# Performance work log

Measured on AMD Instinct MI355X. Metric: run time of the kernel, lower is better.

Reference implementation:

```python
import jax, jax.numpy as jnp
import numpy as np

NUM_QUBITS = 512
NUM_CORES = 16
CORE_SIZE = 64
HIDDEN = 128
BATCH = 2048


def setup_inputs() -> dict:
    key = jax.random.key(0)
    k1, k2, k3 = jax.random.split(key, 3)
    last_assignment = jax.random.randint(k1, (BATCH, NUM_QUBITS), 0, NUM_CORES, dtype=jnp.int32)
    adjacency = jnp.ones((NUM_CORES, NUM_CORES), dtype=jnp.float32)  # all-to-all core graph
    qubit_embedding = jax.random.normal(k2, (NUM_QUBITS + 1, HIDDEN), dtype=jnp.float32)
    gcn_weight = jax.random.normal(k3, (HIDDEN, HIDDEN), dtype=jnp.float32) * (1.0 / np.sqrt(HIDDEN))
    gcn_bias = jnp.zeros((HIDDEN,), dtype=jnp.float32)
    return {
        'last_assignment': last_assignment,
        'adjacency': adjacency,
        'qubit_embedding': qubit_embedding,
        'gcn_weight': gcn_weight,
        'gcn_bias': gcn_bias,
    }


def reference(last_assignment, adjacency, qubit_embedding, gcn_weight, gcn_bias):
    B, Q = last_assignment.shape
    C = adjacency.shape[0]
    # --- replace the sequential per-qubit scatter loop with a single cumsum ---
    # pos[b,q] = number of earlier qubits assigned to the same core (the loop's
    # running counter idx); core index C (the extra row) always writes slot 0
    # because the loop resets its counter every iteration.
    oh = jax.nn.one_hot(last_assignment, C + 1, dtype=jnp.int32)        # [B,Q,C+1]
    cnt = jnp.cumsum(oh, axis=1)                                        # inclusive counts
    pos = jnp.take_along_axis(cnt, last_assignment[..., None], axis=2)[..., 0] - 1
    pos = jnp.where(last_assignment == C, 0, pos)
    buf = jnp.full((B, C + 1, CORE_SIZE), Q, dtype=jnp.int32)           # padding id = num_qubits
    b_idx = jnp.arange(B)[:, None]
    q_idx = jnp.broadcast_to(jnp.arange(Q, dtype=jnp.int32)[None, :], (B, Q))
    buf = buf.at[b_idx, last_assignment, pos].set(q_idx, mode='drop')
    buf = buf[:, :C, :]                                                 # drop overflow core row
    # --- embedding (padding row forced to zero, as nn.Embedding padding_idx) ---
    tbl = qubit_embedding.at[Q].set(0.0)
    qubit_embs = tbl[buf]                                               # [B,C,core_size,H]
    core_embs = qubit_embs.max(axis=2)                                  # [B,C,H]
    # --- GCNConv(add_self_loops=False): D^{-1/2} A D^{-1/2} (X W^T) + b ---
    deg = adjacency.sum(axis=0)
    dinv = jnp.where(deg > 0, 1.0 / jnp.sqrt(deg), 0.0)
    a_norm = adjacency * dinv[:, None] * dinv[None, :]                  # symmetric norm
    h = jnp.einsum('bch,oh->bco', core_embs, gcn_weight)                # lin (PyG: x @ W^T)
    out = jnp.einsum('ij,bjo->bio', a_norm, h) + gcn_bias               # [B,C,H]
    return out
```

## Files before the change

kernel.cpp:

```cpp
#include <hip/hip_runtime.h>
#include <stdint.h>

typedef unsigned short u16;
typedef unsigned int u32;
typedef unsigned long long u64;

typedef __bf16 bf16x8 __attribute__((ext_vector_type(8)));
typedef float f32x4 __attribute__((ext_vector_type(4)));

#define NQ 512
#define NC 16
#define NH 128
#define NB 2048
#define ITEMS 2
#define ESTRIDE 136
#define HSTRIDE 24
#define SENT (-3.0e38f)
#define QE_ELEMS (513*128)

static __device__ __forceinline__ u16 f2bf_rne(float f){
  u32 u = __float_as_uint(f);
  u += 0x7fffu + ((u>>16)&1u);
  return (u16)(u>>16);
}
static __device__ __forceinline__ u32 pack_rne(float lo, float hi){
  return (u32)f2bf_rne(lo) | ((u32)f2bf_rne(hi)<<16);
}
static __device__ __forceinline__ u32 pack_trunc(float lo, float hi){
  return (__float_as_uint(lo)>>16) | (__float_as_uint(hi)&0xffff0000u);
}

union Frag { u32 u[4]; uint4 u4; bf16x8 f; };

__global__ void qe_to_bf16_kernel(const float* __restrict__ qe, u16* __restrict__ wsq)
{
  int i8 = (blockIdx.x * 256 + threadIdx.x) * 8;
  if (i8 + 8 > QE_ELEMS) return;
  const float4* p = (const float4*)(qe + i8);
  float4 a = p[0], b = p[1];
  uint4 o;
  o.x = pack_rne(a.x, a.y); o.y = pack_rne(a.z, a.w);
  o.z = pack_rne(b.x, b.y); o.w = pack_rne(b.z, b.w);
  *(uint4*)(wsq + i8) = o;
}

__global__ __launch_bounds__(256, 4)
void core_snapshot_kernel(const int* __restrict__ la,
                          const float* __restrict__ adj,
                          const u16* __restrict__ qt,
                          const float* __restrict__ gw,
                          const float* __restrict__ gb,
                          float* __restrict__ outp)
{
  __shared__ __align__(16) u16 sE[16*ESTRIDE];
  __shared__ __align__(16) u16 sHB[128*HSTRIDE];
  __shared__ u16 sList[16*64];
  __shared__ u32 sHist[8*16];
  __shared__ u32 sBase[8*16];
  __shared__ u32 sCnt[16];
  __shared__ float sDinv[16];

  const int tid  = threadIdx.x;
  const int lane = tid & 63;
  const int wv   = tid >> 6;
  const int m    = lane & 15;
  const int quad = lane >> 4;

  Frag wfr[2][4];
  #pragma unroll
  for (int t = 0; t < 2; ++t) {
    int o = (wv*2 + t)*16 + m;
    #pragma unroll
    for (int ks = 0; ks < 4; ++ks) {
      const float4* p = (const float4*)(gw + o*NH + ks*32 + quad*8);
      float4 x = p[0], y = p[1];
      wfr[t][ks].u[0] = pack_rne(x.x, x.y);
      wfr[t][ks].u[1] = pack_rne(x.z, x.w);
      wfr[t][ks].u[2] = pack_rne(y.x, y.y);
      wfr[t][ks].u[3] = pack_rne(y.z, y.w);
    }
  }
  if (tid < 16) {
    float s = 0.f;
    for (int i = 0; i < 16; ++i) s += adj[i*16 + tid];
    sDinv[tid] = (s > 0.f) ? (1.0f / sqrtf(s)) : 0.f;
  }
  __syncthreads();

  Frag afr2;
  #pragma unroll
  for (int jj = 0; jj < 4; ++jj) {
    float lo = 0.f, hi = 0.f;
    if (quad < 2) {
      int k0 = quad*8 + jj*2;
      lo = adj[m*16 + k0]     * sDinv[m] * sDinv[k0];
      hi = adj[m*16 + k0 + 1] * sDinv[m] * sDinv[k0 + 1];
    }
    afr2.u[jj] = pack_rne(lo, hi);
  }
  float biasv[2];
  #pragma unroll
  for (int t = 0; t < 2; ++t) biasv[t] = gb[(wv*2 + t)*16 + m];

  const u64 lmask = (1ull << lane) - 1ull;

  for (int it = 0; it < ITEMS; ++it) {
    const int b = blockIdx.x * ITEMS + it;

    int av[2]; u32 intra[2];
    #pragma unroll
    for (int r = 0; r < 2; ++r) {
      int ch = wv*2 + r;
      av[r] = la[b*NQ + ch*64 + lane];
    }
    __syncthreads();
    #pragma unroll
    for (int r = 0; r < 2; ++r) {
      int ch = wv*2 + r;
      #pragma unroll
      for (int c = 0; c < 16; ++c) {
        u64 mk = __ballot(av[r] == c);
        if (lane == c)  sHist[ch*16 + c] = (u32)__popcll(mk);
        if (av[r] == c) intra[r] = (u32)__popcll(mk & lmask);
      }
    }
    __syncthreads();
    if (tid < 16) {
      u32 run = 0;
      #pragma unroll
      for (int ch = 0; ch < 8; ++ch) { sBase[ch*16 + tid] = run; run += sHist[ch*16 + tid]; }
      sCnt[tid] = run;
    }
    __syncthreads();
    #pragma unroll
    for (int r = 0; r < 2; ++r) {
      int ch = wv*2 + r;
      u32 rank = sBase[ch*16 + av[r]] + intra[r];
      if (rank < 64) sList[av[r]*64 + rank] = (u16)(ch*64 + lane);
    }
    __syncthreads();

    {
      const int s0 = quad;
      const int d  = m;
      for (int cc = 0; cc < 4; ++cc) {
        int c = wv*4 + cc;
        int cntc = (int)min(sCnt[c], 64u);
        float a0=SENT,a1=SENT,a2=SENT,a3=SENT,a4=SENT,a5=SENT,a6=SENT,a7=SENT;
        int iters = (cntc + 3) >> 2;
        for (int k = 0; k < iters; ++k) {
          int slot = k*4 + s0;
          bool valid = slot < cntc;
          int qv = valid ? (int)sList[c*64 + slot] : 0;
          uint4 tt = *(const uint4*)(qt + qv*NH + d*8);
          if (!valid) { tt.x = 0xff80ff80u; tt.y = 0xff80ff80u; tt.z = 0xff80ff80u; tt.w = 0xff80ff80u; }
          a0 = fmaxf(a0, __uint_as_float(tt.x << 16));
          a1 = fmaxf(a1, __uint_as_float(tt.x & 0xffff0000u));
          a2 = fmaxf(a2, __uint_as_float(tt.y << 16));
          a3 = fmaxf(a3, __uint_as_float(tt.y & 0xffff0000u));
          a4 = fmaxf(a4, __uint_as_float(tt.z << 16));
          a5 = fmaxf(a5, __uint_as_float(tt.z & 0xffff0000u));
          a6 = fmaxf(a6, __uint_as_float(tt.w << 16));
          a7 = fmaxf(a7, __uint_as_float(tt.w & 0xffff0000u));
        }
        a0 = fmaxf(a0, __shfl_xor(a0, 16)); a0 = fmaxf(a0, __shfl_xor(a0, 32));
        a1 = fmaxf(a1, __shfl_xor(a1, 16)); a1 = fmaxf(a1, __shfl_xor(a1, 32));
        a2 = fmaxf(a2, __shfl_xor(a2, 16)); a2 = fmaxf(a2, __shfl_xor(a2, 32));
        a3 = fmaxf(a3, __shfl_xor(a3, 16)); a3 = fmaxf(a3, __shfl_xor(a3, 32));
        a4 = fmaxf(a4, __shfl_xor(a4, 16)); a4 = fmaxf(a4, __shfl_xor(a4, 32));
        a5 = fmaxf(a5, __shfl_xor(a5, 16)); a5 = fmaxf(a5, __shfl_xor(a5, 32));
        a6 = fmaxf(a6, __shfl_xor(a6, 16)); a6 = fmaxf(a6, __shfl_xor(a6, 32));
        a7 = fmaxf(a7, __shfl_xor(a7, 16)); a7 = fmaxf(a7, __shfl_xor(a7, 32));
        if (cntc < 64) {
          a0=fmaxf(a0,0.f); a1=fmaxf(a1,0.f); a2=fmaxf(a2,0.f); a3=fmaxf(a3,0.f);
          a4=fmaxf(a4,0.f); a5=fmaxf(a5,0.f); a6=fmaxf(a6,0.f); a7=fmaxf(a7,0.f);
        }
        if (quad == 0) {
          uint4 e;
          e.x = pack_trunc(a0,a1); e.y = pack_trunc(a2,a3);
          e.z = pack_trunc(a4,a5); e.w = pack_trunc(a6,a7);
          *(uint4*)&sE[c*ESTRIDE + d*8] = e;
        }
      }
    }
    __syncthreads();

    {
      bf16x8 af[4];
      #pragma unroll
      for (int ks = 0; ks < 4; ++ks)
        af[ks] = *(const bf16x8*)&sE[m*ESTRIDE + ks*32 + quad*8];
      #pragma unroll
      for (int t = 0; t < 2; ++t) {
        int o = (wv*2 + t)*16 + m;
        f32x4 acc = {0.f, 0.f, 0.f, 0.f};
        #pragma unroll
        for (int ks = 0; ks < 4; ++ks)
          acc = __builtin_amdgcn_mfma_f32_16x16x32_bf16(af[ks], wfr[t][ks].f, acc, 0, 0, 0);
        *(u32*)&sHB[o*HSTRIDE + quad*4]     = pack_rne(acc[0], acc[1]);
        *(u32*)&sHB[o*HSTRIDE + quad*4 + 2] = pack_rne(acc[2], acc[3]);
      }
    }
    __syncthreads();

    #pragma unroll
    for (int t = 0; t < 2; ++t) {
      int o = (wv*2 + t)*16 + m;
      Frag bfr;
      if (quad < 2) bfr.u4 = *(const uint4*)&sHB[o*HSTRIDE + quad*8];
      else { bfr.u[0]=0; bfr.u[1]=0; bfr.u[2]=0; bfr.u[3]=0; }
      f32x4 acc = {biasv[t], biasv[t], biasv[t], biasv[t]};
      acc = __builtin_amdgcn_mfma_f32_16x16x32_bf16(afr2.f, bfr.f, acc, 0, 0, 0);
      float* op = outp + b*(NC*NH) + o;
      #pragma unroll
      for (int r = 0; r < 4; ++r) op[(quad*4 + r)*NH] = acc[r];
    }
  }
}

extern "C" void kernel_launch(void* const* d_in, const int* in_sizes, int n_in,
                              void* d_out, int out_size, void* d_ws, size_t ws_size,
                              hipStream_t stream) {
  const int*   la  = (const int*)d_in[0];
  const float* adj = (const float*)d_in[1];
  const float* qe  = (const float*)d_in[2];
  const float* gw  = (const float*)d_in[3];
  const float* gb  = (const float*)d_in[4];
  float* outp = (float*)d_out;
  u16* wsq = (u16*)d_ws;

  qe_to_bf16_kernel<<<(QE_ELEMS/8 + 255)/256, 256, 0, stream>>>(qe, wsq);
  core_snapshot_kernel<<<NB/ITEMS, 256, 0, stream>>>(la, adj, wsq, gw, gb, outp);
}
```

Before: 107.0 us.

## Use order-preserving u16 keys for packed max, one batch per block

The prepass now writes the embedding table as sign-flipped u16 keys, so the gather max runs as packed 16-bit integer max instead of eight float max ops per load. The padding row is written as a zero key, which removes the validity masking in the gather loop. GCN weights are converted to bf16 once in the prepass and read from global memory rather than converted per block. Each block now handles one batch item with launch bounds raised to 8 blocks, trading reuse of the per-block setup for more blocks and higher occupancy.

```diff
diff --git a/kernel.cpp b/kernel.cpp
--- a/kernel.cpp
+++ b/kernel.cpp
@@ -7,16 +7,17 @@
 
 typedef __bf16 bf16x8 __attribute__((ext_vector_type(8)));
 typedef float f32x4 __attribute__((ext_vector_type(4)));
+typedef u16 u16x8 __attribute__((ext_vector_type(8)));
 
 #define NQ 512
 #define NC 16
 #define NH 128
 #define NB 2048
-#define ITEMS 2
 #define ESTRIDE 136
 #define HSTRIDE 24
-#define SENT (-3.0e38f)
-#define QE_ELEMS (513*128)
+#define QE_KEYS (513*128)
+#define WT_OFF  QE_KEYS
+#define GW_ELEMS (128*128)
 
 static __device__ __forceinline__ u16 f2bf_rne(float f){
   u32 u = __float_as_uint(f);
@@ -26,29 +27,51 @@
 static __device__ __forceinline__ u32 pack_rne(float lo, float hi){
   return (u32)f2bf_rne(lo) | ((u32)f2bf_rne(hi)<<16);
 }
-static __device__ __forceinline__ u32 pack_trunc(float lo, float hi){
-  return (__float_as_uint(lo)>>16) | (__float_as_uint(hi)&0xffff0000u);
+static __device__ __forceinline__ u16 key_of(float f){
+  u16 b = f2bf_rne(f);
+  return (b & 0x8000u) ? (u16)~b : (u16)(b | 0x8000u);
+}
+static __device__ __forceinline__ u16 unkey(u16 k){
+  return (k & 0x8000u) ? (u16)(k ^ 0x8000u) : (u16)~k;
 }
 
 union Frag { u32 u[4]; uint4 u4; bf16x8 f; };
-
-__global__ void qe_to_bf16_kernel(const float* __restrict__ qe, u16* __restrict__ wsq)
+union U8   { u16x8 v; int w[4]; uint4 u4; u16 h[8]; };
+
+__global__ void prepass_kernel(const float* __restrict__ qe,
+                               const float* __restrict__ gw,
+                               u16* __restrict__ ws)
 {
-  int i8 = (blockIdx.x * 256 + threadIdx.x) * 8;
-  if (i8 + 8 > QE_ELEMS) return;
-  const float4* p = (const float4*)(qe + i8);
-  float4 a = p[0], b = p[1];
-  uint4 o;
-  o.x = pack_rne(a.x, a.y); o.y = pack_rne(a.z, a.w);
-  o.z = pack_rne(b.x, b.y); o.w = pack_rne(b.z, b.w);
-  *(uint4*)(wsq + i8) = o;
-}
-
-__global__ __launch_bounds__(256, 4)
+  int idx = blockIdx.x * 256 + threadIdx.x;
+  if (idx < QE_KEYS/8) {
+    int i8 = idx * 8;
+    uint4 o;
+    if (i8 >= 512*NH) {
+      o.x = 0x80008000u; o.y = 0x80008000u; o.z = 0x80008000u; o.w = 0x80008000u;
+    } else {
+      const float4* p = (const float4*)(qe + i8);
+      float4 a = p[0], b = p[1];
+      o.x = (u32)key_of(a.x) | ((u32)key_of(a.y)<<16);
+      o.y = (u32)key_of(a.z) | ((u32)key_of(a.w)<<16);
+      o.z = (u32)key_of(b.x) | ((u32)key_of(b.y)<<16);
+      o.w = (u32)key_of(b.z) | ((u32)key_of(b.w)<<16);
+    }
+    *(uint4*)(ws + i8) = o;
+  } else if (idx < QE_KEYS/8 + GW_ELEMS/8) {
+    int j8 = (idx - QE_KEYS/8) * 8;
+    const float4* p = (const float4*)(gw + j8);
+    float4 a = p[0], b = p[1];
+    uint4 o;
+    o.x = pack_rne(a.x, a.y); o.y = pack_rne(a.z, a.w);
+    o.z = pack_rne(b.x, b.y); o.w = pack_rne(b.z, b.w);
+    *(uint4*)(ws + WT_OFF + j8) = o;
+  }
+}
+
+__global__ __launch_bounds__(256, 8)
 void core_snapshot_kernel(const int* __restrict__ la,
                           const float* __restrict__ adj,
-                          const u16* __restrict__ qt,
-                          const float* __restrict__ gw,
+                          const u16* __restrict__ ws,
                           const float* __restrict__ gb,
                           float* __restrict__ outp)
 {
@@ -65,25 +88,98 @@
   const int wv   = tid >> 6;
   const int m    = lane & 15;
   const int quad = lane >> 4;
-
-  Frag wfr[2][4];
-  #pragma unroll
-  for (int t = 0; t < 2; ++t) {
-    int o = (wv*2 + t)*16 + m;
-    #pragma unroll
-    for (int ks = 0; ks < 4; ++ks) {
-      const float4* p = (const float4*)(gw + o*NH + ks*32 + quad*8);
-      float4 x = p[0], y = p[1];
-      wfr[t][ks].u[0] = pack_rne(x.x, x.y);
-      wfr[t][ks].u[1] = pack_rne(x.z, x.w);
-      wfr[t][ks].u[2] = pack_rne(y.x, y.y);
-      wfr[t][ks].u[3] = pack_rne(y.z, y.w);
+  const int b    = blockIdx.x;
+  const u16* qt  = ws;
+  const u16* wt  = ws + WT_OFF;
+
+  int av[2]; u32 intra[2];
+  const u64 lmask = (1ull << lane) - 1ull;
+  #pragma unroll
+  for (int r = 0; r < 2; ++r) {
+    int ch = wv*2 + r;
+    av[r] = la[b*NQ + ch*64 + lane];
+  }
+  #pragma unroll
+  for (int r = 0; r < 2; ++r) {
+    int ch = wv*2 + r;
+    #pragma unroll
+    for (int c = 0; c < 16; ++c) {
+      u64 mk = __ballot(av[r] == c);
+      if (lane == c)  sHist[ch*16 + c] = (u32)__popcll(mk);
+      if (av[r] == c) intra[r] = (u32)__popcll(mk & lmask);
     }
   }
   if (tid < 16) {
     float s = 0.f;
     for (int i = 0; i < 16; ++i) s += adj[i*16 + tid];
     sDinv[tid] = (s > 0.f) ? (1.0f / sqrtf(s)) : 0.f;
+  }
+  __syncthreads();
+  if (tid < 16) {
+    u32 run = 0;
+    #pragma unroll
+    for (int ch = 0; ch < 8; ++ch) { sBase[ch*16 + tid] = run; run += sHist[ch*16 + tid]; }
+    sCnt[tid] = run;
+  }
+  __syncthreads();
+  #pragma unroll
+  for (int r = 0; r < 2; ++r) {
+    int ch = wv*2 + r;
+    u32 rank = sBase[ch*16 + av[r]] + intra[r];
+    if (rank < 64) sList[av[r]*64 + rank] = (u16)(ch*64 + lane);
+  }
+  __syncthreads();
+
+  for (int cc = 0; cc < 4; ++cc) {
+    int c = wv*4 + cc;
+    int cntc = (int)min(sCnt[c], 64u);
+    U8 A; A.v = (u16x8)0;
+    int iters = (cntc + 3) >> 2;
+    for (int k = 0; k < iters; ++k) {
+      int slot = k*4 + quad;
+      int qv = (slot < cntc) ? (int)sList[c*64 + slot] : 512;
+      U8 T; T.u4 = *(const uint4*)(qt + qv*NH + m*8);
+      A.v = __builtin_elementwise_max(A.v, T.v);
+    }
+    U8 Bv;
+    #pragma unroll
+    for (int j = 0; j < 4; ++j) Bv.w[j] = __shfl_xor(A.w[j], 16);
+    A.v = __builtin_elementwise_max(A.v, Bv.v);
+    #pragma unroll
+    for (int j = 0; j < 4; ++j) Bv.w[j] = __shfl_xor(A.w[j], 32);
+    A.v = __builtin_elementwise_max(A.v, Bv.v);
+    if (cntc < 64) {
+      U8 Z; Z.v = (u16x8)(u16)0x8000u;
+      A.v = __builtin_elementwise_max(A.v, Z.v);
+    }
+    if (quad == 0) {
+      uint4 e;
+      e.x = (u32)unkey(A.h[0]) | ((u32)unkey(A.h[1])<<16);
+      e.y = (u32)unkey(A.h[2]) | ((u32)unkey(A.h[3])<<16);
+      e.z = (u32)unkey(A.h[4]) | ((u32)unkey(A.h[5])<<16);
+      e.w = (u32)unkey(A.h[6]) | ((u32)unkey(A.h[7])<<16);
+      *(uint4*)&sE[c*ESTRIDE + m*8] = e;
+    }
+  }
+  __syncthreads();
+
+  {
+    bf16x8 af[4];
+    #pragma unroll
+    for (int ks = 0; ks < 4; ++ks)
+      af[ks] = *(const bf16x8*)&sE[m*ESTRIDE + ks*32 + quad*8];
+    #pragma unroll
+    for (int t = 0; t < 2; ++t) {
+      int o = (wv*2 + t)*16 + m;
+      f32x4 acc = {0.f, 0.f, 0.f, 0.f};
+      #pragma unroll
+      for (int ks = 0; ks < 4; ++ks) {
+        bf16x8 bfr = *(const bf16x8*)(wt + o*NH + ks*32 + quad*8);
+        acc = __builtin_amdgcn_mfma_f32_16x16x32_bf16(af[ks], bfr, acc, 0, 0, 0);
+      }
+      *(u32*)&sHB[o*HSTRIDE + quad*4]     = pack_rne(acc[0], acc[1]);
+      *(u32*)&sHB[o*HSTRIDE + quad*4 + 2] = pack_rne(acc[2], acc[3]);
+    }
   }
   __syncthreads();
 
@@ -98,123 +194,18 @@
     }
     afr2.u[jj] = pack_rne(lo, hi);
   }
-  float biasv[2];
-  #pragma unroll
-  for (int t = 0; t < 2; ++t) biasv[t] = gb[(wv*2 + t)*16 + m];
-
-  const u64 lmask = (1ull << lane) - 1ull;
-
-  for (int it = 0; it < ITEMS; ++it) {
-    const int b = blockIdx.x * ITEMS + it;
-
-    int av[2]; u32 intra[2];
-    #pragma unroll
-    for (int r = 0; r < 2; ++r) {
-      int ch = wv*2 + r;
-      av[r] = la[b*NQ + ch*64 + lane];
-    }
-    __syncthreads();
-    #pragma unroll
-    for (int r = 0; r < 2; ++r) {
-      int ch = wv*2 + r;
-      #pragma unroll
-      for (int c = 0; c < 16; ++c) {
-        u64 mk = __ballot(av[r] == c);
-        if (lane == c)  sHist[ch*16 + c] = (u32)__popcll(mk);
-        if (av[r] == c) intra[r] = (u32)__popcll(mk & lmask);
-      }
-    }
-    __syncthreads();
-    if (tid < 16) {
-      u32 run = 0;
-      #pragma unroll
-      for (int ch = 0; ch < 8; ++ch) { sBase[ch*16 + tid] = run; run += sHist[ch*16 + tid]; }
-      sCnt[tid] = run;
-    }
-    __syncthreads();
-    #pragma unroll
-    for (int r = 0; r < 2; ++r) {
-      int ch = wv*2 + r;
-      u32 rank = sBase[ch*16 + av[r]] + intra[r];
-      if (rank < 64) sList[av[r]*64 + rank] = (u16)(ch*64 + lane);
-    }
-    __syncthreads();
-
-    {
-      const int s0 = quad;
-      const int d  = m;
-      for (int cc = 0; cc < 4; ++cc) {
-        int c = wv*4 + cc;
-        int cntc = (int)min(sCnt[c], 64u);
-        float a0=SENT,a1=SENT,a2=SENT,a3=SENT,a4=SENT,a5=SENT,a6=SENT,a7=SENT;
-        int iters = (cntc + 3) >> 2;
-        for (int k = 0; k < iters; ++k) {
-          int slot = k*4 + s0;
-          bool valid = slot < cntc;
-          int qv = valid ? (int)sList[c*64 + slot] : 0;
-          uint4 tt = *(const uint4*)(qt + qv*NH + d*8);
-          if (!valid) { tt.x = 0xff80ff80u; tt.y = 0xff80ff80u; tt.z = 0xff80ff80u; tt.w = 0xff80ff80u; }
-          a0 = fmaxf(a0, __uint_as_float(tt.x << 16));
-          a1 = fmaxf(a1, __uint_as_float(tt.x & 0xffff0000u));
-          a2 = fmaxf(a2, __uint_as_float(tt.y << 16));
-          a3 = fmaxf(a3, __uint_as_float(tt.y & 0xffff0000u));
-          a4 = fmaxf(a4, __uint_as_float(tt.z << 16));
-          a5 = fmaxf(a5, __uint_as_float(tt.z & 0xffff0000u));
-          a6 = fmaxf(a6, __uint_as_float(tt.w << 16));
-          a7 = fmaxf(a7, __uint_as_float(tt.w & 0xffff0000u));
-        }
-        a0 = fmaxf(a0, __shfl_xor(a0, 16)); a0 = fmaxf(a0, __shfl_xor(a0, 32));
-        a1 = fmaxf(a1, __shfl_xor(a1, 16)); a1 = fmaxf(a1, __shfl_xor(a1, 32));
-        a2 = fmaxf(a2, __shfl_xor(a2, 16)); a2 = fmaxf(a2, __shfl_xor(a2, 32));
-        a3 = fmaxf(a3, __shfl_xor(a3, 16)); a3 = fmaxf(a3, __shfl_xor(a3, 32));
-        a4 = fmaxf(a4, __shfl_xor(a4, 16)); a4 = fmaxf(a4, __shfl_xor(a4, 32));
-        a5 = fmaxf(a5, __shfl_xor(a5, 16)); a5 = fmaxf(a5, __shfl_xor(a5, 32));
-        a6 = fmaxf(a6, __shfl_xor(a6, 16)); a6 = fmaxf(a6, __shfl_xor(a6, 32));
-        a7 = fmaxf(a7, __shfl_xor(a7, 16)); a7 = fmaxf(a7, __shfl_xor(a7, 32));
-        if (cntc < 64) {
-          a0=fmaxf(a0,0.f); a1=fmaxf(a1,0.f); a2=fmaxf(a2,0.f); a3=fmaxf(a3,0.f);
-          a4=fmaxf(a4,0.f); a5=fmaxf(a5,0.f); a6=fmaxf(a6,0.f); a7=fmaxf(a7,0.f);
-        }
-        if (quad == 0) {
-          uint4 e;
-          e.x = pack_trunc(a0,a1); e.y = pack_trunc(a2,a3);
-          e.z = pack_trunc(a4,a5); e.w = pack_trunc(a6,a7);
-          *(uint4*)&sE[c*ESTRIDE + d*8] = e;
-        }
-      }
-    }
-    __syncthreads();
-
-    {
-      bf16x8 af[4];
-      #pragma unroll
-      for (int ks = 0; ks < 4; ++ks)
-        af[ks] = *(const bf16x8*)&sE[m*ESTRIDE + ks*32 + quad*8];
-      #pragma unroll
-      for (int t = 0; t < 2; ++t) {
-        int o = (wv*2 + t)*16 + m;
-        f32x4 acc = {0.f, 0.f, 0.f, 0.f};
-        #pragma unroll
-        for (int ks = 0; ks < 4; ++ks)
-          acc = __builtin_amdgcn_mfma_f32_16x16x32_bf16(af[ks], wfr[t][ks].f, acc, 0, 0, 0);
-        *(u32*)&sHB[o*HSTRIDE + quad*4]     = pack_rne(acc[0], acc[1]);
-        *(u32*)&sHB[o*HSTRIDE + quad*4 + 2] = pack_rne(acc[2], acc[3]);
-      }
-    }
-    __syncthreads();
-
-    #pragma unroll
-    for (int t = 0; t < 2; ++t) {
-      int o = (wv*2 + t)*16 + m;
-      Frag bfr;
-      if (quad < 2) bfr.u4 = *(const uint4*)&sHB[o*HSTRIDE + quad*8];
-      else { bfr.u[0]=0; bfr.u[1]=0; bfr.u[2]=0; bfr.u[3]=0; }
-      f32x4 acc = {biasv[t], biasv[t], biasv[t], biasv[t]};
-      acc = __builtin_amdgcn_mfma_f32_16x16x32_bf16(afr2.f, bfr.f, acc, 0, 0, 0);
-      float* op = outp + b*(NC*NH) + o;
-      #pragma unroll
-      for (int r = 0; r < 4; ++r) op[(quad*4 + r)*NH] = acc[r];
-    }
+  #pragma unroll
+  for (int t = 0; t < 2; ++t) {
+    int o = (wv*2 + t)*16 + m;
+    float biasv = gb[(wv*2 + t)*16 + m];
+    Frag bfr;
+    if (quad < 2) bfr.u4 = *(const uint4*)&sHB[o*HSTRIDE + quad*8];
+    else { bfr.u[0]=0; bfr.u[1]=0; bfr.u[2]=0; bfr.u[3]=0; }
+    f32x4 acc = {biasv, biasv, biasv, biasv};
+    acc = __builtin_amdgcn_mfma_f32_16x16x32_bf16(afr2.f, bfr.f, acc, 0, 0, 0);
+    float* op = outp + b*(NC*NH) + o;
+    #pragma unroll
+    for (int r = 0; r < 4; ++r) op[(quad*4 + r)*NH] = acc[r];
   }
 }
 
@@ -227,8 +218,9 @@
   const float* gw  = (const float*)d_in[3];
   const float* gb  = (const float*)d_in[4];
   float* outp = (float*)d_out;
-  u16* wsq = (u16*)d_ws;
-
-  qe_to_bf16_kernel<<<(QE_ELEMS/8 + 255)/256, 256, 0, stream>>>(qe, wsq);
-  core_snapshot_kernel<<<NB/ITEMS, 256, 0, stream>>>(la, adj, wsq, gw, gb, outp);
-}
+  u16* ws = (u16*)d_ws;
+
+  int pre_threads = QE_KEYS/8 + GW_ELEMS/8;
+  prepass_kernel<<<(pre_threads + 255)/256, 256, 0, stream>>>(qe, gw, ws);
+  core_snapshot_kernel<<<NB, 256, 0, stream>>>(la, adj, ws, gb, outp);
+}
```

Result: faster. 93.92 us (-12.2%).
